# Optimization experiments

Measured on AMD Instinct MI355X. Metric: run time of the kernel, lower is better.

## Reference

```python
import jax, jax.numpy as jnp
import numpy as np

EOS = 1  # EOS_VALUE in the original code (word_label == 1 triggers end_sentence)
L_LAYERS = 2
B, T, H, E = 128, 256, 1024, 1024  # TD == E == input_size


def setup_inputs() -> dict:
    key = jax.random.key(0)
    ks = jax.random.split(key, 20)
    k = 1.0 / np.sqrt(H)
    u = lambda kk, shape: jax.random.uniform(kk, shape, jnp.float32, -k, k)
    inp = {
        "yy_pad": jax.random.randint(ks[0], (B, T), 0, E, dtype=jnp.int32),
        "h_t": jax.random.normal(ks[1], (L_LAYERS, B, H), jnp.float32),
        "h_t_rev": jax.random.normal(ks[2], (L_LAYERS, B, H), jnp.float32),
        "x_lens": jax.random.randint(ks[3], (B,), 1, T - 1, dtype=jnp.int32).at[0].set(T - 1),
        # parameters (layer 0 input size == E == H, so weights stack cleanly)
        "emb": jax.random.normal(ks[4], (E, E), jnp.float32) * 0.02,
        "W_ih": u(ks[5], (L_LAYERS, 4 * H, E)),
        "W_hh": u(ks[6], (L_LAYERS, 4 * H, H)),
        "b_ih": u(ks[7], (L_LAYERS, 4 * H)),
        "b_hh": u(ks[8], (L_LAYERS, 4 * H)),
        "W_ih_rev": u(ks[9], (L_LAYERS, 4 * H, E)),
        "W_hh_rev": u(ks[10], (L_LAYERS, 4 * H, H)),
        "b_ih_rev": u(ks[11], (L_LAYERS, 4 * H)),
        "b_hh_rev": u(ks[12], (L_LAYERS, 4 * H)),
        "c0": jnp.zeros((L_LAYERS, H), jnp.float32),
        "c0_rev": jnp.zeros((L_LAYERS, H), jnp.float32),
        "fc_W": u(ks[13], (E, 2 * H)),
        "fc_b": u(ks[14], (E,)),
    }
    return inp


def _lstm_cell(x, h, c, Wih, Whh, bih, bhh):
    # torch.nn.LSTMCell gate order: input, forget, cell(g), output
    z = x @ Wih.T + bih + h @ Whh.T + bhh  # [B, 4H]
    i, f, g, o = jnp.split(z, 4, axis=-1)
    c2 = jax.nn.sigmoid(f) * c + jax.nn.sigmoid(i) * jnp.tanh(g)
    h2 = jax.nn.sigmoid(o) * jnp.tanh(c2)
    return h2, c2


def reference(yy_pad, h_t, h_t_rev, x_lens, emb, W_ih, W_hh, b_ih, b_hh,
              W_ih_rev, W_hh_rev, b_ih_rev, b_hh_rev, c0, c0_rev, fc_W, fc_b):
    batch = yy_pad.shape[0]
    n_steps = yy_pad.shape[1]  # == max(x_lens) + 1 by construction (static)
    eos_onehot = jax.nn.one_hot(EOS, fc_W.shape[0], dtype=fc_W.dtype)  # [TD]

    c_init = jnp.broadcast_to(c0[:, None, :], (L_LAYERS, batch, c0.shape[1]))
    c_init_rev = jnp.broadcast_to(c0_rev[:, None, :], (L_LAYERS, batch, c0.shape[1]))

    def step(carry, _):
        feed, h, hr, c, cr, ended = carry
        x = emb[feed]   # [B, E]  (sos embedding / previous argmax token)
        xr = x
        hs, hrs, cs, crs = [], [], [], []
        for l in range(L_LAYERS):
            hn, cn = _lstm_cell(x, h[l], c[l], W_ih[l], W_hh[l], b_ih[l], b_hh[l])
            hrn, crn = _lstm_cell(xr, hr[l], cr[l], W_ih_rev[l], W_hh_rev[l], b_ih_rev[l], b_hh_rev[l])
            hs.append(hn); cs.append(cn); hrs.append(hrn); crs.append(crn)
            x, xr = hn, hrn
        h, hr = jnp.stack(hs), jnp.stack(hrs)
        c, cr = jnp.stack(cs), jnp.stack(crs)
        # faithful to torch: cat([B,H],[B,H]) -> [B,2H] -> permute(1,0) -> reshape(B,-1)
        wh = jnp.concatenate([h[-1], hr[-1]], axis=-1).T.reshape(batch, -1)
        logits = wh @ fc_W.T + fc_b  # [B, TD]
        logits = jnp.where(ended[:, None], eos_onehot, logits)
        label = jnp.argmax(logits, axis=1).astype(jnp.int32)
        ended = ended | (label == EOS)
        return (label, h, hr, c, cr, ended), logits

    carry0 = (yy_pad[:, 0], h_t, h_t_rev, c_init, c_init_rev,
              jnp.zeros((batch,), jnp.bool_))
    _, logits_seq = jax.lax.scan(step, carry0, None, length=n_steps)  # [T, B, TD]
    return jax.nn.softmax(jnp.transpose(logits_seq, (1, 0, 2)), axis=-1)  # [B, T, TD]
```

## Files before the change

kernel.cpp:

```cpp
#include <hip/hip_runtime.h>
#include <math.h>

#define NB 128
#define NT 256
#define NH 1024
#define NE 1024
#define G4 4096
#define EOSL 1

#define Z_OFF    ((size_t)0)
#define C_OFF    ((size_t)1048576)
#define HT_OFF   ((size_t)1572864)
#define FCZ_OFF  ((size_t)1835008)
#define BIAS_OFF ((size_t)2883584)
#define END_OFF  ((size_t)2899968)
#define XPH_OFF  ((size_t)2900096)
#define XPX_OFF  ((size_t)3424384)
#define WP_OFF   ((size_t)3555456)
#define TOTAL_MIN_F  ((size_t)3555456)
#define TOTAL_PACK_F ((size_t)37109888)

typedef __attribute__((ext_vector_type(8))) short s8v;
typedef __attribute__((ext_vector_type(4))) float f4v;

struct GMF {
  const float* W[16];
  const unsigned short* Bp[16];
  const unsigned short* Wp[2];
};

__device__ __forceinline__ void add4(float4& d, const float4 a) {
  d.x += a.x; d.y += a.y; d.z += a.z; d.w += a.w;
}
__device__ __forceinline__ float sigmoid_stable(float x) {
  if (x >= 0.f) return 1.f / (1.f + expf(-x));
  float ex = expf(x);
  return ex / (1.f + ex);
}
__device__ __forceinline__ unsigned short bf_rne(float x) {
  unsigned u = __float_as_uint(x);
  return (unsigned short)((u + 0x7FFFu + ((u >> 16) & 1u)) >> 16);
}
__device__ __forceinline__ void split_bf(float x, unsigned short& h, unsigned short& l) {
  unsigned u = __float_as_uint(x);
  unsigned hb = (u + 0x7FFFu + ((u >> 16) & 1u)) >> 16;
  h = (unsigned short)hb;
  float r = x - __uint_as_float(hb << 16);
  l = bf_rne(r);
}
__device__ __forceinline__ void cvt8(float4 a0, float4 a1, s8v& hi, s8v& lo)
{
  const float v[8] = {a0.x, a0.y, a0.z, a0.w, a1.x, a1.y, a1.z, a1.w};
  #pragma unroll
  for (int j = 0; j < 8; j++) {
    unsigned short h, l; split_bf(v[j], h, l);
    hi[j] = (short)h; lo[j] = (short)l;
  }
}


__global__ void k_init(const int* yy, const float* h_t, const float* h_tr,
                       const float* c0, const float* c0r,
                       const float* b_ih, const float* b_hh,
                       const float* b_ihr, const float* b_hhr,
                       const float* emb,
                       unsigned short* xph, unsigned short* xpx,
                       float* call, float* bias, int* ended)
{
  int idx = blockIdx.x * 256 + threadIdx.x;
  if (idx < 2 * 2048 * 128) {
    int dir = idx / (2048 * 128); int rem = idx % (2048 * 128);
    int row = rem >> 7, b = rem & 127;
    int l = row >> 10, n = row & 1023;
    const float* src = dir ? h_tr : h_t;
    float v = src[((size_t)l * 128 + b) * 1024 + n];
    unsigned short h, lo; split_bf(v, h, lo);
    size_t off = ((size_t)(dir * 64 + (row >> 5)) * 8 + (b >> 4)) * 1024
               + ((b & 15) + 16 * ((n >> 3) & 3)) * 8 + (n & 7);
    xph[off] = h; xph[off + 512] = lo;
  }
  if (idx < 4 * 1024 * 128) {
    int ld = idx / (1024 * 128); int l = ld >> 1, dir = ld & 1;
    int rem = idx % (1024 * 128); int n = rem >> 7;
    call[idx] = (dir ? c0r : c0)[l * 1024 + n];
  }
  if (idx < 4 * 4096) {
    int ld = idx / 4096; int l = ld >> 1, dir = ld & 1;
    int m = idx & 4095;
    bias[idx] = (dir ? b_ihr : b_ih)[l * 4096 + m] + (dir ? b_hhr : b_hh)[l * 4096 + m];
  }
  if (idx < 128 * 1024) {
    int b = idx >> 10, k = idx & 1023;
    int e = yy[b * NT];
    float v = emb[(size_t)e * 1024 + k];
    unsigned short h, lo; split_bf(v, h, lo);
    size_t off = ((size_t)(k >> 5) * 8 + (b >> 4)) * 1024
               + ((b & 15) + 16 * ((k >> 3) & 3)) * 8 + (k & 7);
    xpx[off] = h; xpx[off + 512] = lo;
  }
  if (idx < NB) ended[idx] = 0;
}

__global__ void k_packW(const float* W_ih, const float* W_hh,
                        const float* W_ihr, const float* W_hhr,
                        unsigned short* WP)
{
  int idx = blockIdx.x * 256 + threadIdx.x;
  int l = idx & 63;
  int frag = idx >> 6;
  int ktile = frag & 63;
  int mtile = (frag >> 6) & 255;
  int ld = frag >> 14;
  int layer = ld >> 1, dir = ld & 1;
  int m = mtile * 16 + (l & 15);
  int kg = ktile * 32 + (l >> 4) * 8;
  const float* base;
  if (kg < 1024) base = (dir ? W_ihr : W_ih) + ((size_t)layer * 4096 + m) * 1024 + kg;
  else           base = (dir ? W_hhr : W_hh) + ((size_t)layer * 4096 + m) * 1024 + (kg - 1024);
  float4 a0 = *(const float4*)base, a1 = *(const float4*)(base + 4);
  s8v hi, lo; cvt8(a0, a1, hi, lo);
  unsigned short* outp = WP + (size_t)frag * 1024 + l * 8;
  *(s8v*)outp = hi;
  *(s8v*)(outp + 512) = lo;
}

__device__ __forceinline__ void red_write(float* red, int slot, int l, const f4v (&acc)[2][8])
{
  #pragma unroll
  for (int mt = 0; mt < 2; mt++)
    #pragma unroll
    for (int bt = 0; bt < 8; bt++)
      *(f4v*)&red[(size_t)slot * 4096 + (mt * 8 + bt) * 256 + l * 4] = acc[mt][bt];
}
__device__ __forceinline__ void red_add(const float* red, int slot, int l, f4v (&acc)[2][8])
{
  #pragma unroll
  for (int mt = 0; mt < 2; mt++)
    #pragma unroll
    for (int bt = 0; bt < 8; bt++)
      acc[mt][bt] += *(const f4v*)&red[(size_t)slot * 4096 + (mt * 8 + bt) * 256 + l * 4];
}

template<int PACKED>
__global__ __launch_bounds__(512, 2) void k_gemm(GMF d, float* z)
{
  const int mb = blockIdx.x, dir = blockIdx.y;
  const int tid = threadIdx.x, l = tid & 63, w = tid >> 6;
  const int m0 = mb * 32;
  const int lr = l & 15, lk = l >> 4;
  __shared__ __align__(16) float red[4 * 4096];

  f4v acc[2][8];
  #pragma unroll
  for (int mt = 0; mt < 2; mt++)
    #pragma unroll
    for (int bt = 0; bt < 8; bt++)
      acc[mt][bt] = (f4v)(0.0f);

  const unsigned short* Bb = d.Bp[dir * 8 + w] + l * 8;

  if (PACKED) {
    const unsigned short* Wb = d.Wp[dir]
        + (((size_t)(mb * 2) * 64 + w * 8) << 10) + l * 8;
    s8v whc[2], wlc[2];
    #pragma unroll
    for (int mt = 0; mt < 2; mt++) {
      const unsigned short* p = Wb + ((size_t)(mt * 64) << 10);
      whc[mt] = *(const s8v*)p; wlc[mt] = *(const s8v*)(p + 512);
    }
    #pragma unroll 1
    for (int kk = 0; kk < 8; kk++) {
      s8v bh[8], bl[8];
      #pragma unroll
      for (int bt = 0; bt < 8; bt++) {
        const unsigned short* p = Bb + ((size_t)(kk * 8 + bt) << 10);
        bh[bt] = *(const s8v*)p; bl[bt] = *(const s8v*)(p + 512);
      }
      s8v whn[2], wln[2];
      if (kk < 7) {
        #pragma unroll
        for (int mt = 0; mt < 2; mt++) {
          const unsigned short* p = Wb + ((size_t)(mt * 64 + kk + 1) << 10);
          whn[mt] = *(const s8v*)p; wln[mt] = *(const s8v*)(p + 512);
        }
      }
      #pragma unroll
      for (int mt = 0; mt < 2; mt++)
        #pragma unroll
        for (int bt = 0; bt < 8; bt++) {
          acc[mt][bt] = __builtin_amdgcn_mfma_f32_16x16x32_bf16(whc[mt], bh[bt], acc[mt][bt], 0, 0, 0);
          acc[mt][bt] = __builtin_amdgcn_mfma_f32_16x16x32_bf16(whc[mt], bl[bt], acc[mt][bt], 0, 0, 0);
          acc[mt][bt] = __builtin_amdgcn_mfma_f32_16x16x32_bf16(wlc[mt], bh[bt], acc[mt][bt], 0, 0, 0);
        }
      if (kk < 7) {
        whc[0] = whn[0]; whc[1] = whn[1];
        wlc[0] = wln[0]; wlc[1] = wln[1];
      }
    }
  } else {
    const float* Wb = d.W[dir * 8 + w] + (size_t)(m0 + lr) * 1024 + lk * 8;
    float4 ac[2][2];
    #pragma unroll
    for (int mt = 0; mt < 2; mt++) {
      ac[mt][0] = *(const float4*)(Wb + (size_t)mt * 16384);
      ac[mt][1] = *(const float4*)(Wb + (size_t)mt * 16384 + 4);
    }
    #pragma unroll 1
    for (int kk = 0; kk < 8; kk++) {
      s8v bh[8], bl[8];
      #pragma unroll
      for (int bt = 0; bt < 8; bt++) {
        const unsigned short* p = Bb + ((size_t)(kk * 8 + bt) << 10);
        bh[bt] = *(const s8v*)p; bl[bt] = *(const s8v*)(p + 512);
      }
      float4 an[2][2];
      if (kk < 7) {
        #pragma unroll
        for (int mt = 0; mt < 2; mt++) {
          an[mt][0] = *(const float4*)(Wb + (size_t)mt * 16384 + (kk + 1) * 32);
          an[mt][1] = *(const float4*)(Wb + (size_t)mt * 16384 + (kk + 1) * 32 + 4);
        }
      }
      #pragma unroll
      for (int mt = 0; mt < 2; mt++) {
        s8v wh, wl;
        cvt8(ac[mt][0], ac[mt][1], wh, wl);
        #pragma unroll
        for (int bt = 0; bt < 8; bt++) {
          acc[mt][bt] = __builtin_amdgcn_mfma_f32_16x16x32_bf16(wh, bh[bt], acc[mt][bt], 0, 0, 0);
          acc[mt][bt] = __builtin_amdgcn_mfma_f32_16x16x32_bf16(wh, bl[bt], acc[mt][bt], 0, 0, 0);
          acc[mt][bt] = __builtin_amdgcn_mfma_f32_16x16x32_bf16(wl, bh[bt], acc[mt][bt], 0, 0, 0);
        }
      }
      if (kk < 7) {
        #pragma unroll
        for (int mt = 0; mt < 2; mt++) { ac[mt][0] = an[mt][0]; ac[mt][1] = an[mt][1]; }
      }
    }
  }

  if (w >= 4) red_write(red, w - 4, l, acc);
  __syncthreads();
  if (w < 4) red_add(red, w, l, acc);
  __syncthreads();
  if (w == 2 || w == 3) red_write(red, w - 2, l, acc);
  __syncthreads();
  if (w < 2) red_add(red, w, l, acc);
  __syncthreads();
  if (w < 2) red_write(red, w, l, acc);
  __syncthreads();
  float* zb = z + (size_t)dir * 4096 * 128;
  #pragma unroll
  for (int vi = 0; vi < 2; vi++) {
    int v = tid + vi * 512;
    f4v s = *(const f4v*)&red[(size_t)v * 4];
    s += *(const f4v*)&red[(size_t)4096 + (size_t)v * 4];
    int frag = v >> 6, lane = v & 63;
    int mt = frag >> 3, bt = frag & 7;
    int m = m0 + mt * 16 + (lane >> 4) * 4;
    int b = bt * 16 + (lane & 15);
    #pragma unroll
    for (int r = 0; r < 4; r++)
      zb[(size_t)(m + r) * 128 + b] = s[r];
  }
}

__global__ void k_gates(const float* z, const float* bias, float* c,
                        unsigned short* xph, int ktile0, float* hB)
{
  int t = threadIdx.x;
  int idx = blockIdx.x * 256 + t;
  int n = idx >> 5, cc = (idx & 31) << 2;
  int dir = blockIdx.y;
  float4 g[4];
  #pragma unroll
  for (int gg = 0; gg < 4; gg++) {
    int row = gg * 1024 + n;
    float4 s = *(const float4*)(z + ((size_t)dir * 4096 + row) * 128 + cc);
    float b = bias[dir * 4096 + row];
    s.x += b; s.y += b; s.z += b; s.w += b;
    g[gg] = s;
  }
  float* cp = c + ((size_t)dir * 1024 + n) * 128 + cc;
  float4 cold = *(float4*)cp;
  float4 cn, hn;
  cn.x = sigmoid_stable(g[1].x) * cold.x + sigmoid_stable(g[0].x) * tanhf(g[2].x);
  cn.y = sigmoid_stable(g[1].y) * cold.y + sigmoid_stable(g[0].y) * tanhf(g[2].y);
  cn.z = sigmoid_stable(g[1].z) * cold.z + sigmoid_stable(g[0].z) * tanhf(g[2].z);
  cn.w = sigmoid_stable(g[1].w) * cold.w + sigmoid_stable(g[0].w) * tanhf(g[2].w);
  hn.x = sigmoid_stable(g[3].x) * tanhf(cn.x);
  hn.y = sigmoid_stable(g[3].y) * tanhf(cn.y);
  hn.z = sigmoid_stable(g[3].z) * tanhf(cn.z);
  hn.w = sigmoid_stable(g[3].w) * tanhf(cn.w);
  *(float4*)cp = cn;
  size_t fo = ((size_t)(dir * 64 + ktile0 + (n >> 5)) * 8 + (cc >> 4)) * 1024
            + ((cc & 15) + 16 * ((n >> 3) & 3)) * 8 + (n & 7);
  const float* hv = &hn.x;
  #pragma unroll
  for (int j = 0; j < 4; j++) {
    unsigned short h, lo; split_bf(hv[j], h, lo);
    xph[fo + j * 8] = h;
    xph[fo + j * 8 + 512] = lo;
  }
  if (hB)
    *(float4*)(hB + (size_t)dir * (1024 * 128) + (size_t)n * 128 + cc) = hn;
}

__global__ __launch_bounds__(256) void k_fc(const float* Ht, const float* fc_W, float* fcz)
{
  int et = blockIdx.x, kp = blockIdx.y;
  int e0 = et * 64;
  int k00 = kp * 256;
  __shared__ __align__(16) float in_s[128][36];
  __shared__ __align__(16) float w_s[64][36];
  int t = threadIdx.x, e_sub = t & 7, bg = t >> 3, b0 = bg * 4;
  float acc[8][4] = {};
  for (int kc = 0; kc < 256; kc += 32) {
    #pragma unroll
    for (int i = 0; i < 4; i++) {
      int flat = t + 256 * i, r = flat >> 3, f4i = flat & 7;
      const float* row = Ht + (r >= 64 ? (size_t)NH * NB + (size_t)(r - 64) * 2048
                                       : (size_t)r * 2048);
      float4 v = *(const float4*)(row + k00 + kc + f4i * 4);
      int sw = (f4i ^ (r >> 2)) & 7;
      *(float4*)&in_s[r][sw * 4] = v;
    }
    #pragma unroll
    for (int i = 0; i < 2; i++) {
      int flat = t + 256 * i, r = flat >> 3, f4i = flat & 7;
      *(float4*)&w_s[r][f4i * 4] =
          *(const float4*)(fc_W + (size_t)(e0 + r) * 2048 + k00 + kc + f4i * 4);
    }
    __syncthreads();
    #pragma unroll
    for (int kq = 0; kq < 8; kq++) {
      int ksw = (kq ^ bg) & 7;
      float4 a4[4];
      #pragma unroll
      for (int ib = 0; ib < 4; ib++) a4[ib] = *(const float4*)&in_s[b0 + ib][ksw * 4];
      float4 w4[8];
      #pragma unroll
      for (int je = 0; je < 8; je++) w4[je] = *(const float4*)&w_s[e_sub + 8 * je][kq * 4];
      #pragma unroll
      for (int je = 0; je < 8; je++)
        #pragma unroll
        for (int ib = 0; ib < 4; ib++)
          acc[je][ib] += a4[ib].x * w4[je].x + a4[ib].y * w4[je].y +
                         a4[ib].z * w4[je].z + a4[ib].w * w4[je].w;
    }
    __syncthreads();
  }
  for (int je = 0; je < 8; je++) {
    int e = e0 + e_sub + 8 * je;
    for (int ib = 0; ib < 4; ib++)
      fcz[((size_t)kp * NB + b0 + ib) * NE + e] = acc[je][ib];
  }
}

__global__ void k_final(const float* fcz, const float* fc_b, int* ended,
                        float* out, int tstep, const float* emb, unsigned short* xpx)
{
  int b = blockIdx.x;
  int t = threadIdx.x;
  __shared__ float sval[256];
  __shared__ int   sidx[256];
  __shared__ float ssum[256];
  bool end = (ended[b] != 0);
  float v[4];
  int e_base = t * 4;
  float4 vv = *(const float4*)&fc_b[e_base];
  #pragma unroll
  for (int p = 0; p < 8; p++)
    add4(vv, *(const float4*)&fcz[((size_t)p * NB + b) * NE + e_base]);
  v[0] = vv.x; v[1] = vv.y; v[2] = vv.z; v[3] = vv.w;
  if (end) {
    #pragma unroll
    for (int j = 0; j < 4; j++) v[j] = (e_base + j == EOSL) ? 1.f : 0.f;
  }
  float bv = v[0]; int bi = e_base;
  #pragma unroll
  for (int j = 1; j < 4; j++) if (v[j] > bv) { bv = v[j]; bi = e_base + j; }
  sval[t] = bv; sidx[t] = bi;
  __syncthreads();
  for (int s = 128; s > 0; s >>= 1) {
    if (t < s) {
      float ov = sval[t + s]; int oi = sidx[t + s];
      if (ov > sval[t] || (ov == sval[t] && oi < sidx[t])) { sval[t] = ov; sidx[t] = oi; }
    }
    __syncthreads();
  }
  float m = sval[0]; int label = sidx[0];
  {
    int k0 = t * 4;
    float4 e4 = *(const float4*)(emb + (size_t)label * 1024 + k0);
    size_t off = ((size_t)(k0 >> 5) * 8 + (b >> 4)) * 1024
               + ((b & 15) + 16 * ((k0 >> 3) & 3)) * 8 + (k0 & 7);
    ushort4 h4, l4;
    unsigned short hh, ll;
    split_bf(e4.x, hh, ll); h4.x = hh; l4.x = ll;
    split_bf(e4.y, hh, ll); h4.y = hh; l4.y = ll;
    split_bf(e4.z, hh, ll); h4.z = hh; l4.z = ll;
    split_bf(e4.w, hh, ll); h4.w = hh; l4.w = ll;
    *(ushort4*)(xpx + off) = h4;
    *(ushort4*)(xpx + off + 512) = l4;
  }
  float ls = 0.f;
  #pragma unroll
  for (int j = 0; j < 4; j++) { v[j] = expf(v[j] - m); ls += v[j]; }
  ssum[t] = ls;
  __syncthreads();
  for (int s = 128; s > 0; s >>= 1) { if (t < s) ssum[t] += ssum[t + s]; __syncthreads(); }
  float inv = 1.f / ssum[0];
  float* orow = out + ((size_t)b * NT + tstep) * NE + e_base;
  #pragma unroll
  for (int j = 0; j < 4; j++) orow[j] = v[j] * inv;
  if (t == 0) ended[b] = (end || label == EOSL) ? 1 : 0;
}

extern "C" void kernel_launch(void* const* d_in, const int* in_sizes, int n_in,
                              void* d_out, int out_size, void* d_ws, size_t ws_size,
                              hipStream_t stream)
{
  const int*   yy    = (const int*)d_in[0];
  const float* h_t   = (const float*)d_in[1];
  const float* h_tr  = (const float*)d_in[2];
  const float* emb   = (const float*)d_in[4];
  const float* W_ih  = (const float*)d_in[5];
  const float* W_hh  = (const float*)d_in[6];
  const float* b_ih  = (const float*)d_in[7];
  const float* b_hh  = (const float*)d_in[8];
  const float* W_ihr = (const float*)d_in[9];
  const float* W_hhr = (const float*)d_in[10];
  const float* b_ihr = (const float*)d_in[11];
  const float* b_hhr = (const float*)d_in[12];
  const float* c0    = (const float*)d_in[13];
  const float* c0r   = (const float*)d_in[14];
  const float* fc_W  = (const float*)d_in[15];
  const float* fc_b  = (const float*)d_in[16];
  float* out = (float*)d_out;

  float* ws   = (float*)d_ws;
  float* z    = ws + Z_OFF;
  float* call = ws + C_OFF;
  float* Ht   = ws + HT_OFF;
  float* fcz  = ws + FCZ_OFF;
  float* bias = ws + BIAS_OFF;
  int* ended  = (int*)(ws + END_OFF);
  unsigned short* xph = (unsigned short*)(ws + XPH_OFF);
  unsigned short* xpx = (unsigned short*)(ws + XPX_OFF);
  unsigned short* WP  = (unsigned short*)(ws + WP_OFF);
  bool packed = ws_size >= TOTAL_PACK_F * sizeof(float);

  k_init<<<2048, 256, 0, stream>>>(yy, h_t, h_tr, c0, c0r, b_ih, b_hh, b_ihr, b_hhr,
                                   emb, xph, xpx, call, bias, ended);
  if (packed)
    k_packW<<<16384, 256, 0, stream>>>(W_ih, W_hh, W_ihr, W_hhr, WP);

  GMF d0, d1;
  for (int dir = 0; dir < 2; dir++) {
    const float* Wih0 = dir ? W_ihr : W_ih;
    const float* Whh0 = dir ? W_hhr : W_hh;
    const float* Wih1 = Wih0 + (size_t)G4 * NH;
    const float* Whh1 = Whh0 + (size_t)G4 * NH;
    for (int ks = 0; ks < 8; ks++) {
      d0.W[dir * 8 + ks]  = (ks < 4) ? (Wih0 + ks * 256) : (Whh0 + (ks - 4) * 256);
      d0.Bp[dir * 8 + ks] = (ks < 4) ? (xpx + (size_t)(ks * 64) * 1024)
                                     : (xph + (size_t)((dir * 64 + (ks - 4) * 8) * 8) * 1024);
      d1.W[dir * 8 + ks]  = (ks < 4) ? (Wih1 + ks * 256) : (Whh1 + (ks - 4) * 256);
      d1.Bp[dir * 8 + ks] = xph + (size_t)((dir * 64 + ks * 8) * 8) * 1024;
    }
    d0.Wp[dir] = WP + (size_t)(0 * 2 + dir) * 256 * 64 * 1024;
    d1.Wp[dir] = WP + (size_t)(1 * 2 + dir) * 256 * 64 * 1024;
  }

  for (int t = 0; t < NT; t++) {
    if (packed) k_gemm<1><<<dim3(128, 2), 512, 0, stream>>>(d0, z);
    else        k_gemm<0><<<dim3(128, 2), 512, 0, stream>>>(d0, z);
    k_gates<<<dim3(128, 2), 256, 0, stream>>>(z, bias, call, xph, 0, nullptr);
    if (packed) k_gemm<1><<<dim3(128, 2), 512, 0, stream>>>(d1, z);
    else        k_gemm<0><<<dim3(128, 2), 512, 0, stream>>>(d1, z);
    k_gates<<<dim3(128, 2), 256, 0, stream>>>(z, bias + 2 * 4096,
                                              call + (size_t)2 * 1024 * 128, xph, 32, Ht);
    k_fc<<<dim3(16, 8), 256, 0, stream>>>(Ht, fc_W, fcz);
    k_final<<<128, 256, 0, stream>>>(fcz, fc_b, ended, out, t, emb, xpx);
  }
}
```

Measured before the change: 23.95 ms.

## Fuse per-step LSTM kernels into one persistent kernel with grid barriers

The six kernel launches per timestep (two GEMMs, two gate kernels, FC, final softmax) become one persistent 256-block kernel that loops over timesteps and synchronises through an atomic grid barrier. Weights are repacked so each block owns all four gates for 8 hidden units, which lets the gate nonlinearity run in the GEMM epilogue and removes the z round-trip through global memory. The hidden-state buffer is double-buffered by step parity. This removes about 1500 launches and their gaps, but relies on all 256 blocks being co-resident, adds spin-barrier cost, and the barrier's bounded spin can break out early and silently corrupt results.

```diff
diff --git a/kernel.cpp b/kernel.cpp
--- a/kernel.cpp
+++ b/kernel.cpp
@@ -8,30 +8,21 @@
 #define G4 4096
 #define EOSL 1
 
-#define Z_OFF    ((size_t)0)
-#define C_OFF    ((size_t)1048576)
-#define HT_OFF   ((size_t)1572864)
-#define FCZ_OFF  ((size_t)1835008)
+#define C_OFF    ((size_t)0)
+#define HT_OFF   ((size_t)524288)
+#define FCZ_OFF  ((size_t)786432)
 #define BIAS_OFF ((size_t)2883584)
 #define END_OFF  ((size_t)2899968)
-#define XPH_OFF  ((size_t)2900096)
-#define XPX_OFF  ((size_t)3424384)
-#define WP_OFF   ((size_t)3555456)
-#define TOTAL_MIN_F  ((size_t)3555456)
-#define TOTAL_PACK_F ((size_t)37109888)
+#define BAR_OFF  ((size_t)2900096)
+#define XPH_OFF  ((size_t)2900160)
+#define XPX_OFF  ((size_t)3948736)
+#define WP_OFF   ((size_t)4079808)
+#define TOTAL_MIN_F  ((size_t)4079808)
+#define TOTAL_PACK_F ((size_t)37634240)
 
 typedef __attribute__((ext_vector_type(8))) short s8v;
 typedef __attribute__((ext_vector_type(4))) float f4v;
 
-struct GMF {
-  const float* W[16];
-  const unsigned short* Bp[16];
-  const unsigned short* Wp[2];
-};
-
-__device__ __forceinline__ void add4(float4& d, const float4 a) {
-  d.x += a.x; d.y += a.y; d.z += a.z; d.w += a.w;
-}
 __device__ __forceinline__ float sigmoid_stable(float x) {
   if (x >= 0.f) return 1.f / (1.f + expf(-x));
   float ex = expf(x);
@@ -59,13 +50,36 @@
 }
 
 
+__device__ __forceinline__ void gbar(int* cnt, int* gen, int& mygen)
+{
+  __syncthreads();
+  if (threadIdx.x == 0) {
+    __threadfence();
+    int target = mygen + 1;
+    if (__hip_atomic_fetch_add(cnt, 1, __ATOMIC_ACQ_REL, __HIP_MEMORY_SCOPE_AGENT)
+        == (int)gridDim.x - 1) {
+      __hip_atomic_store(cnt, 0, __ATOMIC_RELAXED, __HIP_MEMORY_SCOPE_AGENT);
+      __hip_atomic_fetch_add(gen, 1, __ATOMIC_RELEASE, __HIP_MEMORY_SCOPE_AGENT);
+    } else {
+      int guard = 0;
+      while (__hip_atomic_load(gen, __ATOMIC_ACQUIRE, __HIP_MEMORY_SCOPE_AGENT) < target) {
+        __builtin_amdgcn_s_sleep(2);
+        if (++guard > (1 << 20)) break;
+      }
+    }
+    mygen = target;
+    __threadfence();
+  }
+  __syncthreads();
+}
+
 __global__ void k_init(const int* yy, const float* h_t, const float* h_tr,
                        const float* c0, const float* c0r,
                        const float* b_ih, const float* b_hh,
                        const float* b_ihr, const float* b_hhr,
                        const float* emb,
                        unsigned short* xph, unsigned short* xpx,
-                       float* call, float* bias, int* ended)
+                       float* call, float* bias, int* ended, int* bar)
 {
   int idx = blockIdx.x * 256 + threadIdx.x;
   if (idx < 2 * 2048 * 128) {
@@ -99,6 +113,7 @@
     xpx[off] = h; xpx[off + 512] = lo;
   }
   if (idx < NB) ended[idx] = 0;
+  if (idx < 2) bar[idx] = 0;
 }
 
 __global__ void k_packW(const float* W_ih, const float* W_hh,
@@ -112,7 +127,10 @@
   int mtile = (frag >> 6) & 255;
   int ld = frag >> 14;
   int layer = ld >> 1, dir = ld & 1;
-  int m = mtile * 16 + (l & 15);
+  int s = l & 15;
+  int mbb = mtile >> 1, half = mtile & 1;
+  int gate = half * 2 + (s >> 3);
+  int m = gate * 1024 + mbb * 8 + (s & 7);
   int kg = ktile * 32 + (l >> 4) * 8;
   const float* base;
   if (kg < 1024) base = (dir ? W_ihr : W_ih) + ((size_t)layer * 4096 + m) * 1024 + kg;
@@ -141,280 +159,276 @@
       acc[mt][bt] += *(const f4v*)&red[(size_t)slot * 4096 + (mt * 8 + bt) * 256 + l * 4];
 }
 
+struct KP {
+  const unsigned short* WP;
+  const float* Wih; const float* Whh; const float* Wihr; const float* Whhr;
+  const float* bias; float* c; float* Ht; float* fcz;
+  unsigned short* xph; unsigned short* xpx;
+  const float* fcW; const float* fcb; const float* emb;
+  float* out; int* ended; int* bar;
+};
+
 template<int PACKED>
-__global__ __launch_bounds__(512, 2) void k_gemm(GMF d, float* z)
-{
-  const int mb = blockIdx.x, dir = blockIdx.y;
-  const int tid = threadIdx.x, l = tid & 63, w = tid >> 6;
-  const int m0 = mb * 32;
+__global__ __launch_bounds__(512, 2) void k_all(KP p)
+{
+  __shared__ __align__(16) float lds[16384];
+  const int bid = blockIdx.x, tid = threadIdx.x;
+  const int l = tid & 63, w = tid >> 6;
+  const int dir = bid >> 7, mb = bid & 127;
   const int lr = l & 15, lk = l >> 4;
-  __shared__ __align__(16) float red[4 * 4096];
-
-  f4v acc[2][8];
-  #pragma unroll
-  for (int mt = 0; mt < 2; mt++)
-    #pragma unroll
-    for (int bt = 0; bt < 8; bt++)
-      acc[mt][bt] = (f4v)(0.0f);
-
-  const unsigned short* Bb = d.Bp[dir * 8 + w] + l * 8;
-
-  if (PACKED) {
-    const unsigned short* Wb = d.Wp[dir]
-        + (((size_t)(mb * 2) * 64 + w * 8) << 10) + l * 8;
-    s8v whc[2], wlc[2];
-    #pragma unroll
-    for (int mt = 0; mt < 2; mt++) {
-      const unsigned short* p = Wb + ((size_t)(mt * 64) << 10);
-      whc[mt] = *(const s8v*)p; wlc[mt] = *(const s8v*)(p + 512);
+  int mygen = 0;
+
+  for (int t = 0; t < NT; t++) {
+    unsigned short* xpR = p.xph + (size_t)(t & 1) * 1048576;
+    unsigned short* xpW = p.xph + (size_t)((t & 1) ^ 1) * 1048576;
+
+    for (int layer = 0; layer < 2; layer++) {
+      const unsigned short* Bb;
+      if (layer == 0)
+        Bb = (w < 4) ? p.xpx + (size_t)w * 65536
+                     : xpR + (size_t)(dir * 64 + (w - 4) * 8) * 8192;
+      else
+        Bb = (w < 4) ? xpW + (size_t)(dir * 64 + w * 8) * 8192
+                     : xpR + (size_t)(dir * 64 + 32 + (w - 4) * 8) * 8192;
+      Bb += l * 8;
+
+      f4v acc[2][8];
+      #pragma unroll
+      for (int mt = 0; mt < 2; mt++)
+        #pragma unroll
+        for (int bt = 0; bt < 8; bt++)
+          acc[mt][bt] = (f4v)(0.0f);
+
+      if (PACKED) {
+        const unsigned short* Wb = p.WP + (size_t)(layer * 2 + dir) * 16777216ULL
+            + (((size_t)(mb * 2) * 64 + (size_t)w * 8) << 10) + l * 8;
+        s8v whc[2], wlc[2];
+        #pragma unroll
+        for (int mt = 0; mt < 2; mt++) {
+          const unsigned short* q = Wb + ((size_t)(mt * 64) << 10);
+          whc[mt] = *(const s8v*)q; wlc[mt] = *(const s8v*)(q + 512);
+        }
+        #pragma unroll 1
+        for (int kk = 0; kk < 8; kk++) {
+          s8v bh[8], bl[8];
+          #pragma unroll
+          for (int bt = 0; bt < 8; bt++) {
+            const unsigned short* q = Bb + ((size_t)(kk * 8 + bt) << 10);
+            bh[bt] = *(const s8v*)q; bl[bt] = *(const s8v*)(q + 512);
+          }
+          s8v whn[2], wln[2];
+          if (kk < 7) {
+            #pragma unroll
+            for (int mt = 0; mt < 2; mt++) {
+              const unsigned short* q = Wb + ((size_t)(mt * 64 + kk + 1) << 10);
+              whn[mt] = *(const s8v*)q; wln[mt] = *(const s8v*)(q + 512);
+            }
+          }
+          #pragma unroll
+          for (int mt = 0; mt < 2; mt++)
+            #pragma unroll
+            for (int bt = 0; bt < 8; bt++) {
+              acc[mt][bt] = __builtin_amdgcn_mfma_f32_16x16x32_bf16(whc[mt], bh[bt], acc[mt][bt], 0, 0, 0);
+              acc[mt][bt] = __builtin_amdgcn_mfma_f32_16x16x32_bf16(whc[mt], bl[bt], acc[mt][bt], 0, 0, 0);
+              acc[mt][bt] = __builtin_amdgcn_mfma_f32_16x16x32_bf16(wlc[mt], bh[bt], acc[mt][bt], 0, 0, 0);
+            }
+          if (kk < 7) {
+            whc[0] = whn[0]; whc[1] = whn[1];
+            wlc[0] = wln[0]; wlc[1] = wln[1];
+          }
+        }
+      } else {
+        const float* Wsel = ((w < 4) ? (dir ? p.Wihr : p.Wih) : (dir ? p.Whhr : p.Whh))
+                          + (size_t)layer * 4194304;
+        int col0 = (w & 3) * 256 + lk * 8;
+        const float* Wrow[2];
+        Wrow[0] = Wsel + ((size_t)(((lr >> 3)) * 1024 + mb * 8 + (lr & 7))) * 1024 + col0;
+        Wrow[1] = Wsel + ((size_t)((2 + (lr >> 3)) * 1024 + mb * 8 + (lr & 7))) * 1024 + col0;
+        float4 ac[2][2];
+        #pragma unroll
+        for (int mt = 0; mt < 2; mt++) {
+          ac[mt][0] = *(const float4*)(Wrow[mt]);
+          ac[mt][1] = *(const float4*)(Wrow[mt] + 4);
+        }
+        #pragma unroll 1
+        for (int kk = 0; kk < 8; kk++) {
+          s8v bh[8], bl[8];
+          #pragma unroll
+          for (int bt = 0; bt < 8; bt++) {
+            const unsigned short* q = Bb + ((size_t)(kk * 8 + bt) << 10);
+            bh[bt] = *(const s8v*)q; bl[bt] = *(const s8v*)(q + 512);
+          }
+          float4 an[2][2];
+          if (kk < 7) {
+            #pragma unroll
+            for (int mt = 0; mt < 2; mt++) {
+              an[mt][0] = *(const float4*)(Wrow[mt] + (kk + 1) * 32);
+              an[mt][1] = *(const float4*)(Wrow[mt] + (kk + 1) * 32 + 4);
+            }
+          }
+          #pragma unroll
+          for (int mt = 0; mt < 2; mt++) {
+            s8v wh, wl;
+            cvt8(ac[mt][0], ac[mt][1], wh, wl);
+            #pragma unroll
+            for (int bt = 0; bt < 8; bt++) {
+              acc[mt][bt] = __builtin_amdgcn_mfma_f32_16x16x32_bf16(wh, bh[bt], acc[mt][bt], 0, 0, 0);
+              acc[mt][bt] = __builtin_amdgcn_mfma_f32_16x16x32_bf16(wh, bl[bt], acc[mt][bt], 0, 0, 0);
+              acc[mt][bt] = __builtin_amdgcn_mfma_f32_16x16x32_bf16(wl, bh[bt], acc[mt][bt], 0, 0, 0);
+            }
+          }
+          if (kk < 7) {
+            #pragma unroll
+            for (int mt = 0; mt < 2; mt++) { ac[mt][0] = an[mt][0]; ac[mt][1] = an[mt][1]; }
+          }
+        }
+      }
+
+      if (w >= 4) red_write(lds, w - 4, l, acc);
+      __syncthreads();
+      if (w < 4) red_add(lds, w, l, acc);
+      __syncthreads();
+      if (w == 2 || w == 3) red_write(lds, w - 2, l, acc);
+      __syncthreads();
+      if (w < 2) red_add(lds, w, l, acc);
+      __syncthreads();
+      if (w < 2) red_write(lds, w, l, acc);
+      __syncthreads();
+      float* zs = lds + 8192;
+      #pragma unroll
+      for (int vi = 0; vi < 2; vi++) {
+        int v = tid + vi * 512;
+        f4v s = *(const f4v*)&lds[(size_t)v * 4];
+        s += *(const f4v*)&lds[4096 + (size_t)v * 4];
+        int frag = v >> 6, lane = v & 63;
+        int mt = frag >> 3, bt = frag & 7;
+        int s0 = (lane >> 4) * 4, bcol = bt * 16 + (lane & 15);
+        #pragma unroll
+        for (int r = 0; r < 4; r++)
+          zs[mt * 2048 + (s0 + r) * 128 + bcol] = s[r];
+      }
+      __syncthreads();
+
+      int ld = layer * 2 + dir;
+      #pragma unroll
+      for (int half = 0; half < 2; half++) {
+        int cell = tid + half * 512;
+        int nl = cell >> 7, b = cell & 127;
+        int n = mb * 8 + nl;
+        float iv = zs[nl * 128 + b]              + p.bias[ld * 4096 + n];
+        float fv = zs[(nl + 8) * 128 + b]        + p.bias[ld * 4096 + 1024 + n];
+        float gv = zs[2048 + nl * 128 + b]       + p.bias[ld * 4096 + 2048 + n];
+        float ov = zs[2048 + (nl + 8) * 128 + b] + p.bias[ld * 4096 + 3072 + n];
+        float* cp = p.c + ((size_t)ld * 1024 + n) * 128 + b;
+        float cold = *cp;
+        float cn = sigmoid_stable(fv) * cold + sigmoid_stable(iv) * tanhf(gv);
+        float hn = sigmoid_stable(ov) * tanhf(cn);
+        *cp = cn;
+        int kt = layer * 32 + (n >> 5), n5 = n & 31;
+        size_t off = ((size_t)(dir * 64 + kt) * 8 + (b >> 4)) * 1024
+                   + ((b & 15) + 16 * ((n5 >> 3) & 3)) * 8 + (n5 & 7);
+        unsigned short hh, lo; split_bf(hn, hh, lo);
+        xpW[off] = hh; xpW[off + 512] = lo;
+        if (layer == 1)
+          p.Ht[(size_t)dir * 131072 + (size_t)n * 128 + b] = hn;
+      }
+      gbar(p.bar, p.bar + 1, mygen);
     }
-    #pragma unroll 1
-    for (int kk = 0; kk < 8; kk++) {
-      s8v bh[8], bl[8];
-      #pragma unroll
-      for (int bt = 0; bt < 8; bt++) {
-        const unsigned short* p = Bb + ((size_t)(kk * 8 + bt) << 10);
-        bh[bt] = *(const s8v*)p; bl[bt] = *(const s8v*)(p + 512);
-      }
-      s8v whn[2], wln[2];
-      if (kk < 7) {
-        #pragma unroll
-        for (int mt = 0; mt < 2; mt++) {
-          const unsigned short* p = Wb + ((size_t)(mt * 64 + kk + 1) << 10);
-          whn[mt] = *(const s8v*)p; wln[mt] = *(const s8v*)(p + 512);
-        }
-      }
-      #pragma unroll
-      for (int mt = 0; mt < 2; mt++)
-        #pragma unroll
-        for (int bt = 0; bt < 8; bt++) {
-          acc[mt][bt] = __builtin_amdgcn_mfma_f32_16x16x32_bf16(whc[mt], bh[bt], acc[mt][bt], 0, 0, 0);
-          acc[mt][bt] = __builtin_amdgcn_mfma_f32_16x16x32_bf16(whc[mt], bl[bt], acc[mt][bt], 0, 0, 0);
-          acc[mt][bt] = __builtin_amdgcn_mfma_f32_16x16x32_bf16(wlc[mt], bh[bt], acc[mt][bt], 0, 0, 0);
-        }
-      if (kk < 7) {
-        whc[0] = whn[0]; whc[1] = whn[1];
-        wlc[0] = wln[0]; wlc[1] = wln[1];
-      }
+
+    {
+      int et = bid & 15, kp = bid >> 4;
+      int e0 = et * 64, k00 = kp * 128;
+      float* in_s = lds;
+      float* w_s  = lds + 4608;
+      int e_sub = tid & 7, bg = tid >> 3, b0 = bg * 2;
+      float accf[8][2];
+      #pragma unroll
+      for (int je = 0; je < 8; je++) { accf[je][0] = 0.f; accf[je][1] = 0.f; }
+      for (int kc = 0; kc < 128; kc += 32) {
+        #pragma unroll
+        for (int i = 0; i < 2; i++) {
+          int flat = tid + 512 * i, r = flat >> 3, f4i = flat & 7;
+          float4 v = *(const float4*)(p.Ht + (size_t)r * 2048 + k00 + kc + f4i * 4);
+          int sw = (f4i ^ (r >> 2)) & 7;
+          *(float4*)&in_s[r * 36 + sw * 4] = v;
+        }
+        {
+          int r = tid >> 3, f4i = tid & 7;
+          *(float4*)&w_s[r * 36 + f4i * 4] =
+              *(const float4*)(p.fcW + (size_t)(e0 + r) * 2048 + k00 + kc + f4i * 4);
+        }
+        __syncthreads();
+        #pragma unroll
+        for (int kq = 0; kq < 8; kq++) {
+          int ksw = (kq ^ (bg >> 1)) & 7;
+          float4 a0 = *(const float4*)&in_s[b0 * 36 + ksw * 4];
+          float4 a1 = *(const float4*)&in_s[(b0 + 1) * 36 + ksw * 4];
+          #pragma unroll
+          for (int je = 0; je < 8; je++) {
+            float4 w4 = *(const float4*)&w_s[(e_sub + 8 * je) * 36 + kq * 4];
+            accf[je][0] += a0.x * w4.x + a0.y * w4.y + a0.z * w4.z + a0.w * w4.w;
+            accf[je][1] += a1.x * w4.x + a1.y * w4.y + a1.z * w4.z + a1.w * w4.w;
+          }
+        }
+        __syncthreads();
+      }
+      #pragma unroll
+      for (int je = 0; je < 8; je++) {
+        int e = e0 + e_sub + 8 * je;
+        p.fcz[((size_t)kp * 128 + b0) * 1024 + e]     = accf[je][0];
+        p.fcz[((size_t)kp * 128 + b0 + 1) * 1024 + e] = accf[je][1];
+      }
+      gbar(p.bar, p.bar + 1, mygen);
     }
-  } else {
-    const float* Wb = d.W[dir * 8 + w] + (size_t)(m0 + lr) * 1024 + lk * 8;
-    float4 ac[2][2];
-    #pragma unroll
-    for (int mt = 0; mt < 2; mt++) {
-      ac[mt][0] = *(const float4*)(Wb + (size_t)mt * 16384);
-      ac[mt][1] = *(const float4*)(Wb + (size_t)mt * 16384 + 4);
+
+    if (bid < 128) {
+      int b = bid;
+      float* sval = lds;
+      int*   sidx = (int*)(lds + 512);
+      float* ssum = lds + 1024;
+      bool end = (p.ended[b] != 0);
+      int e2 = tid * 2;
+      float vx = p.fcb[e2], vy = p.fcb[e2 + 1];
+      #pragma unroll
+      for (int q = 0; q < 16; q++) {
+        const float* f = &p.fcz[((size_t)q * 128 + b) * 1024 + e2];
+        vx += f[0]; vy += f[1];
+      }
+      if (end) { vx = (e2 == EOSL) ? 1.f : 0.f; vy = (e2 + 1 == EOSL) ? 1.f : 0.f; }
+      float bv; int bi;
+      if (vy > vx) { bv = vy; bi = e2 + 1; } else { bv = vx; bi = e2; }
+      sval[tid] = bv; sidx[tid] = bi;
+      __syncthreads();
+      for (int s = 256; s > 0; s >>= 1) {
+        if (tid < s) {
+          float ov = sval[tid + s]; int oi = sidx[tid + s];
+          if (ov > sval[tid] || (ov == sval[tid] && oi < sidx[tid])) { sval[tid] = ov; sidx[tid] = oi; }
+        }
+        __syncthreads();
+      }
+      float m = sval[0]; int label = sidx[0];
+      {
+        int k0 = tid * 2;
+        float ex = p.emb[(size_t)label * 1024 + k0];
+        float ey = p.emb[(size_t)label * 1024 + k0 + 1];
+        size_t off = ((size_t)(k0 >> 5) * 8 + (b >> 4)) * 1024
+                   + ((b & 15) + 16 * ((k0 >> 3) & 3)) * 8 + (k0 & 7);
+        unsigned short h0, l0, h1, l1;
+        split_bf(ex, h0, l0); split_bf(ey, h1, l1);
+        p.xpx[off] = h0; p.xpx[off + 1] = h1;
+        p.xpx[off + 512] = l0; p.xpx[off + 513] = l1;
+      }
+      float ex0 = expf(vx - m), ex1 = expf(vy - m);
+      ssum[tid] = ex0 + ex1;
+      __syncthreads();
+      for (int s = 256; s > 0; s >>= 1) { if (tid < s) ssum[tid] += ssum[tid + s]; __syncthreads(); }
+      float inv = 1.f / ssum[0];
+      float* orow = p.out + ((size_t)b * NT + t) * NE + e2;
+      orow[0] = ex0 * inv; orow[1] = ex1 * inv;
+      if (tid == 0) p.ended[b] = (end || label == EOSL) ? 1 : 0;
     }
-    #pragma unroll 1
-    for (int kk = 0; kk < 8; kk++) {
-      s8v bh[8], bl[8];
-      #pragma unroll
-      for (int bt = 0; bt < 8; bt++) {
-        const unsigned short* p = Bb + ((size_t)(kk * 8 + bt) << 10);
-        bh[bt] = *(const s8v*)p; bl[bt] = *(const s8v*)(p + 512);
-      }
-      float4 an[2][2];
-      if (kk < 7) {
-        #pragma unroll
-        for (int mt = 0; mt < 2; mt++) {
-          an[mt][0] = *(const float4*)(Wb + (size_t)mt * 16384 + (kk + 1) * 32);
-          an[mt][1] = *(const float4*)(Wb + (size_t)mt * 16384 + (kk + 1) * 32 + 4);
-        }
-      }
-      #pragma unroll
-      for (int mt = 0; mt < 2; mt++) {
-        s8v wh, wl;
-        cvt8(ac[mt][0], ac[mt][1], wh, wl);
-        #pragma unroll
-        for (int bt = 0; bt < 8; bt++) {
-          acc[mt][bt] = __builtin_amdgcn_mfma_f32_16x16x32_bf16(wh, bh[bt], acc[mt][bt], 0, 0, 0);
-          acc[mt][bt] = __builtin_amdgcn_mfma_f32_16x16x32_bf16(wh, bl[bt], acc[mt][bt], 0, 0, 0);
-          acc[mt][bt] = __builtin_amdgcn_mfma_f32_16x16x32_bf16(wl, bh[bt], acc[mt][bt], 0, 0, 0);
-        }
-      }
-      if (kk < 7) {
-        #pragma unroll
-        for (int mt = 0; mt < 2; mt++) { ac[mt][0] = an[mt][0]; ac[mt][1] = an[mt][1]; }
-      }
-    }
-  }
-
-  if (w >= 4) red_write(red, w - 4, l, acc);
-  __syncthreads();
-  if (w < 4) red_add(red, w, l, acc);
-  __syncthreads();
-  if (w == 2 || w == 3) red_write(red, w - 2, l, acc);
-  __syncthreads();
-  if (w < 2) red_add(red, w, l, acc);
-  __syncthreads();
-  if (w < 2) red_write(red, w, l, acc);
-  __syncthreads();
-  float* zb = z + (size_t)dir * 4096 * 128;
-  #pragma unroll
-  for (int vi = 0; vi < 2; vi++) {
-    int v = tid + vi * 512;
-    f4v s = *(const f4v*)&red[(size_t)v * 4];
-    s += *(const f4v*)&red[(size_t)4096 + (size_t)v * 4];
-    int frag = v >> 6, lane = v & 63;
-    int mt = frag >> 3, bt = frag & 7;
-    int m = m0 + mt * 16 + (lane >> 4) * 4;
-    int b = bt * 16 + (lane & 15);
-    #pragma unroll
-    for (int r = 0; r < 4; r++)
-      zb[(size_t)(m + r) * 128 + b] = s[r];
-  }
-}
-
-__global__ void k_gates(const float* z, const float* bias, float* c,
-                        unsigned short* xph, int ktile0, float* hB)
-{
-  int t = threadIdx.x;
-  int idx = blockIdx.x * 256 + t;
-  int n = idx >> 5, cc = (idx & 31) << 2;
-  int dir = blockIdx.y;
-  float4 g[4];
-  #pragma unroll
-  for (int gg = 0; gg < 4; gg++) {
-    int row = gg * 1024 + n;
-    float4 s = *(const float4*)(z + ((size_t)dir * 4096 + row) * 128 + cc);
-    float b = bias[dir * 4096 + row];
-    s.x += b; s.y += b; s.z += b; s.w += b;
-    g[gg] = s;
-  }
-  float* cp = c + ((size_t)dir * 1024 + n) * 128 + cc;
-  float4 cold = *(float4*)cp;
-  float4 cn, hn;
-  cn.x = sigmoid_stable(g[1].x) * cold.x + sigmoid_stable(g[0].x) * tanhf(g[2].x);
-  cn.y = sigmoid_stable(g[1].y) * cold.y + sigmoid_stable(g[0].y) * tanhf(g[2].y);
-  cn.z = sigmoid_stable(g[1].z) * cold.z + sigmoid_stable(g[0].z) * tanhf(g[2].z);
-  cn.w = sigmoid_stable(g[1].w) * cold.w + sigmoid_stable(g[0].w) * tanhf(g[2].w);
-  hn.x = sigmoid_stable(g[3].x) * tanhf(cn.x);
-  hn.y = sigmoid_stable(g[3].y) * tanhf(cn.y);
-  hn.z = sigmoid_stable(g[3].z) * tanhf(cn.z);
-  hn.w = sigmoid_stable(g[3].w) * tanhf(cn.w);
-  *(float4*)cp = cn;
-  size_t fo = ((size_t)(dir * 64 + ktile0 + (n >> 5)) * 8 + (cc >> 4)) * 1024
-            + ((cc & 15) + 16 * ((n >> 3) & 3)) * 8 + (n & 7);
-  const float* hv = &hn.x;
-  #pragma unroll
-  for (int j = 0; j < 4; j++) {
-    unsigned short h, lo; split_bf(hv[j], h, lo);
-    xph[fo + j * 8] = h;
-    xph[fo + j * 8 + 512] = lo;
-  }
-  if (hB)
-    *(float4*)(hB + (size_t)dir * (1024 * 128) + (size_t)n * 128 + cc) = hn;
-}
-
-__global__ __launch_bounds__(256) void k_fc(const float* Ht, const float* fc_W, float* fcz)
-{
-  int et = blockIdx.x, kp = blockIdx.y;
-  int e0 = et * 64;
-  int k00 = kp * 256;
-  __shared__ __align__(16) float in_s[128][36];
-  __shared__ __align__(16) float w_s[64][36];
-  int t = threadIdx.x, e_sub = t & 7, bg = t >> 3, b0 = bg * 4;
-  float acc[8][4] = {};
-  for (int kc = 0; kc < 256; kc += 32) {
-    #pragma unroll
-    for (int i = 0; i < 4; i++) {
-      int flat = t + 256 * i, r = flat >> 3, f4i = flat & 7;
-      const float* row = Ht + (r >= 64 ? (size_t)NH * NB + (size_t)(r - 64) * 2048
-                                       : (size_t)r * 2048);
-      float4 v = *(const float4*)(row + k00 + kc + f4i * 4);
-      int sw = (f4i ^ (r >> 2)) & 7;
-      *(float4*)&in_s[r][sw * 4] = v;
-    }
-    #pragma unroll
-    for (int i = 0; i < 2; i++) {
-      int flat = t + 256 * i, r = flat >> 3, f4i = flat & 7;
-      *(float4*)&w_s[r][f4i * 4] =
-          *(const float4*)(fc_W + (size_t)(e0 + r) * 2048 + k00 + kc + f4i * 4);
-    }
-    __syncthreads();
-    #pragma unroll
-    for (int kq = 0; kq < 8; kq++) {
-      int ksw = (kq ^ bg) & 7;
-      float4 a4[4];
-      #pragma unroll
-      for (int ib = 0; ib < 4; ib++) a4[ib] = *(const float4*)&in_s[b0 + ib][ksw * 4];
-      float4 w4[8];
-      #pragma unroll
-      for (int je = 0; je < 8; je++) w4[je] = *(const float4*)&w_s[e_sub + 8 * je][kq * 4];
-      #pragma unroll
-      for (int je = 0; je < 8; je++)
-        #pragma unroll
-        for (int ib = 0; ib < 4; ib++)
-          acc[je][ib] += a4[ib].x * w4[je].x + a4[ib].y * w4[je].y +
-                         a4[ib].z * w4[je].z + a4[ib].w * w4[je].w;
-    }
-    __syncthreads();
-  }
-  for (int je = 0; je < 8; je++) {
-    int e = e0 + e_sub + 8 * je;
-    for (int ib = 0; ib < 4; ib++)
-      fcz[((size_t)kp * NB + b0 + ib) * NE + e] = acc[je][ib];
-  }
-}
-
-__global__ void k_final(const float* fcz, const float* fc_b, int* ended,
-                        float* out, int tstep, const float* emb, unsigned short* xpx)
-{
-  int b = blockIdx.x;
-  int t = threadIdx.x;
-  __shared__ float sval[256];
-  __shared__ int   sidx[256];
-  __shared__ float ssum[256];
-  bool end = (ended[b] != 0);
-  float v[4];
-  int e_base = t * 4;
-  float4 vv = *(const float4*)&fc_b[e_base];
-  #pragma unroll
-  for (int p = 0; p < 8; p++)
-    add4(vv, *(const float4*)&fcz[((size_t)p * NB + b) * NE + e_base]);
-  v[0] = vv.x; v[1] = vv.y; v[2] = vv.z; v[3] = vv.w;
-  if (end) {
-    #pragma unroll
-    for (int j = 0; j < 4; j++) v[j] = (e_base + j == EOSL) ? 1.f : 0.f;
-  }
-  float bv = v[0]; int bi = e_base;
-  #pragma unroll
-  for (int j = 1; j < 4; j++) if (v[j] > bv) { bv = v[j]; bi = e_base + j; }
-  sval[t] = bv; sidx[t] = bi;
-  __syncthreads();
-  for (int s = 128; s > 0; s >>= 1) {
-    if (t < s) {
-      float ov = sval[t + s]; int oi = sidx[t + s];
-      if (ov > sval[t] || (ov == sval[t] && oi < sidx[t])) { sval[t] = ov; sidx[t] = oi; }
-    }
-    __syncthreads();
-  }
-  float m = sval[0]; int label = sidx[0];
-  {
-    int k0 = t * 4;
-    float4 e4 = *(const float4*)(emb + (size_t)label * 1024 + k0);
-    size_t off = ((size_t)(k0 >> 5) * 8 + (b >> 4)) * 1024
-               + ((b & 15) + 16 * ((k0 >> 3) & 3)) * 8 + (k0 & 7);
-    ushort4 h4, l4;
-    unsigned short hh, ll;
-    split_bf(e4.x, hh, ll); h4.x = hh; l4.x = ll;
-    split_bf(e4.y, hh, ll); h4.y = hh; l4.y = ll;
-    split_bf(e4.z, hh, ll); h4.z = hh; l4.z = ll;
-    split_bf(e4.w, hh, ll); h4.w = hh; l4.w = ll;
-    *(ushort4*)(xpx + off) = h4;
-    *(ushort4*)(xpx + off + 512) = l4;
-  }
-  float ls = 0.f;
-  #pragma unroll
-  for (int j = 0; j < 4; j++) { v[j] = expf(v[j] - m); ls += v[j]; }
-  ssum[t] = ls;
-  __syncthreads();
-  for (int s = 128; s > 0; s >>= 1) { if (t < s) ssum[t] += ssum[t + s]; __syncthreads(); }
-  float inv = 1.f / ssum[0];
-  float* orow = out + ((size_t)b * NT + tstep) * NE + e_base;
-  #pragma unroll
-  for (int j = 0; j < 4; j++) orow[j] = v[j] * inv;
-  if (t == 0) ended[b] = (end || label == EOSL) ? 1 : 0;
+    gbar(p.bar, p.bar + 1, mygen);
+  }
 }
 
 extern "C" void kernel_launch(void* const* d_in, const int* in_sizes, int n_in,
@@ -439,49 +453,29 @@
   const float* fc_b  = (const float*)d_in[16];
   float* out = (float*)d_out;
 
-  float* ws   = (float*)d_ws;
-  float* z    = ws + Z_OFF;
-  float* call = ws + C_OFF;
-  float* Ht   = ws + HT_OFF;
-  float* fcz  = ws + FCZ_OFF;
-  float* bias = ws + BIAS_OFF;
-  int* ended  = (int*)(ws + END_OFF);
-  unsigned short* xph = (unsigned short*)(ws + XPH_OFF);
-  unsigned short* xpx = (unsigned short*)(ws + XPX_OFF);
-  unsigned short* WP  = (unsigned short*)(ws + WP_OFF);
+  float* ws = (float*)d_ws;
+  KP p;
+  p.c     = ws + C_OFF;
+  p.Ht    = ws + HT_OFF;
+  p.fcz   = ws + FCZ_OFF;
+  p.bias  = ws + BIAS_OFF;
+  p.ended = (int*)(ws + END_OFF);
+  p.bar   = (int*)(ws + BAR_OFF);
+  p.xph   = (unsigned short*)(ws + XPH_OFF);
+  p.xpx   = (unsigned short*)(ws + XPX_OFF);
+  p.WP    = (const unsigned short*)(ws + WP_OFF);
+  p.Wih = W_ih; p.Whh = W_hh; p.Wihr = W_ihr; p.Whhr = W_hhr;
+  p.fcW = fc_W; p.fcb = fc_b; p.emb = emb;
+  p.out = out;
   bool packed = ws_size >= TOTAL_PACK_F * sizeof(float);
 
   k_init<<<2048, 256, 0, stream>>>(yy, h_t, h_tr, c0, c0r, b_ih, b_hh, b_ihr, b_hhr,
-                                   emb, xph, xpx, call, bias, ended);
+                                   emb, p.xph, p.xpx, p.c, (float*)p.bias,
+                                   p.ended, p.bar);
   if (packed)
-    k_packW<<<16384, 256, 0, stream>>>(W_ih, W_hh, W_ihr, W_hhr, WP);
-
-  GMF d0, d1;
-  for (int dir = 0; dir < 2; dir++) {
-    const float* Wih0 = dir ? W_ihr : W_ih;
-    const float* Whh0 = dir ? W_hhr : W_hh;
-    const float* Wih1 = Wih0 + (size_t)G4 * NH;
-    const float* Whh1 = Whh0 + (size_t)G4 * NH;
-    for (int ks = 0; ks < 8; ks++) {
-      d0.W[dir * 8 + ks]  = (ks < 4) ? (Wih0 + ks * 256) : (Whh0 + (ks - 4) * 256);
-      d0.Bp[dir * 8 + ks] = (ks < 4) ? (xpx + (size_t)(ks * 64) * 1024)
-                                     : (xph + (size_t)((dir * 64 + (ks - 4) * 8) * 8) * 1024);
-      d1.W[dir * 8 + ks]  = (ks < 4) ? (Wih1 + ks * 256) : (Whh1 + (ks - 4) * 256);
-      d1.Bp[dir * 8 + ks] = xph + (size_t)((dir * 64 + ks * 8) * 8) * 1024;
-    }
-    d0.Wp[dir] = WP + (size_t)(0 * 2 + dir) * 256 * 64 * 1024;
-    d1.Wp[dir] = WP + (size_t)(1 * 2 + dir) * 256 * 64 * 1024;
-  }
-
-  for (int t = 0; t < NT; t++) {
-    if (packed) k_gemm<1><<<dim3(128, 2), 512, 0, stream>>>(d0, z);
-    else        k_gemm<0><<<dim3(128, 2), 512, 0, stream>>>(d0, z);
-    k_gates<<<dim3(128, 2), 256, 0, stream>>>(z, bias, call, xph, 0, nullptr);
-    if (packed) k_gemm<1><<<dim3(128, 2), 512, 0, stream>>>(d1, z);
-    else        k_gemm<0><<<dim3(128, 2), 512, 0, stream>>>(d1, z);
-    k_gates<<<dim3(128, 2), 256, 0, stream>>>(z, bias + 2 * 4096,
-                                              call + (size_t)2 * 1024 * 128, xph, 32, Ht);
-    k_fc<<<dim3(16, 8), 256, 0, stream>>>(Ht, fc_W, fcz);
-    k_final<<<128, 256, 0, stream>>>(fcz, fc_b, ended, out, t, emb, xpx);
-  }
-}
+    k_packW<<<16384, 256, 0, stream>>>(W_ih, W_hh, W_ihr, W_hhr,
+                                       (unsigned short*)p.WP);
+
+  if (packed) k_all<1><<<256, 512, 0, stream>>>(p);
+  else        k_all<0><<<256, 512, 0, stream>>>(p);
+}
```

After: 79.36 ms. 3.31x slower.
